# Kernel optimization log

Measured on AMD Instinct MI355X. Metric: run time of the kernel, lower is better.

## Reference

```python
import jax, jax.numpy as jnp
import numpy as np

B, N, F_DIM, E, C = 8, 16384, 64, 262144, 10
BN_EPS = 1e-5


def setup_inputs() -> dict:
    key = jax.random.key(0)
    ks = jax.random.split(key, 10)
    s = 1.0 / np.sqrt(F_DIM)
    return {
        "x": jax.random.normal(ks[0], (B, N, F_DIM), jnp.float32),
        "edge_src": jax.random.randint(ks[1], (B, E), 0, N, jnp.int32),
        "edge_dst": jax.random.randint(ks[2], (B, E), 0, N, jnp.int32),
        "W1": jax.random.normal(ks[3], (F_DIM, F_DIM), jnp.float32) * s,
        "b1": jax.random.normal(ks[4], (F_DIM,), jnp.float32) * 0.01,
        "W2": jax.random.normal(ks[5], (F_DIM, F_DIM), jnp.float32) * s,
        "b2": jax.random.normal(ks[6], (F_DIM,), jnp.float32) * 0.01,
        "bn_gamma": jnp.ones((F_DIM,), jnp.float32),
        "bn_beta": jnp.zeros((F_DIM,), jnp.float32),
        "lin_W": jax.random.normal(ks[7], (C, N * F_DIM), jnp.float32) * (1.0 / np.sqrt(N * F_DIM)),
        "lin_b": jax.random.normal(ks[8], (C,), jnp.float32) * 0.01,
    }


def _graph_conv(x, src, dst, W, b):
    # DGL GraphConv, norm='both', in_feats == out_feats (aggregate-first path):
    # h = D_in^{-1/2} * A * (D_out^{-1/2} * x) @ W + b, degrees clamped to >= 1.
    ones = jnp.ones((src.shape[0],), x.dtype)
    deg_out = jnp.maximum(jax.ops.segment_sum(ones, src, num_segments=N), 1.0)
    deg_in = jnp.maximum(jax.ops.segment_sum(ones, dst, num_segments=N), 1.0)
    xs = x * jax.lax.rsqrt(deg_out)[:, None]          # [N, F]
    agg = jax.ops.segment_sum(xs[src], dst, num_segments=N)  # gather + scatter-add
    rst = agg * jax.lax.rsqrt(deg_in)[:, None]
    return rst @ W + b


def reference(x, edge_src, edge_dst, W1, b1, W2, b2, bn_gamma, bn_beta, lin_W, lin_b):
    conv = jax.vmap(_graph_conv, in_axes=(0, 0, 0, None, None))
    h = jax.nn.relu(conv(x, edge_src, edge_dst, W1, b1))  # conv1 + relu
    # dropout p=0.0 (eval): identity
    h = conv(h, edge_src, edge_dst, W2, b2)               # conv2 -> [B, N, F]
    # BatchNorm1d over channel F (torch normalizes over B and N in training mode)
    mean = jnp.mean(h, axis=(0, 1))
    var = jnp.var(h, axis=(0, 1))
    h = bn_gamma * (h - mean) * jax.lax.rsqrt(var + BN_EPS) + bn_beta
    flat = h.reshape(B, N * F_DIM)
    return flat @ lin_W.T + lin_b                         # [B, C]
```

## Files before the change

### kernel.cpp

```cpp
#include <hip/hip_runtime.h>

#define B_     8
#define N_     16384
#define F_     64
#define E_     262144
#define C_     10
#define NF_    (N_ * F_)
#define BN_    (B_ * N_)
#define BNF_   (B_ * N_ * F_)
#define BE_    (B_ * E_)
#define CAP_   48
#define CHUNK_ 8192
#define NCH_   (E_ / CHUNK_)
#define NW_    (N_ / 4)
#define NSB_   4096
#define NFB_   1024
#define EPS_   1e-5f

typedef _Float16 h8 __attribute__((ext_vector_type(8)));
typedef _Float16 h4 __attribute__((ext_vector_type(4)));
typedef float f32x4 __attribute__((ext_vector_type(4)));

#define SWZ(r, o) ((((r) * 64 + (o))) ^ (((r) & 7) << 3))

__global__ __launch_bounds__(256) void k_count(const int* __restrict__ src,
                                               const int* __restrict__ dst,
                                               unsigned int* __restrict__ partO,
                                               unsigned int* __restrict__ partI,
                                               const float* __restrict__ W1,
                                               const float* __restrict__ W2,
                                               _Float16* __restrict__ Wt1,
                                               _Float16* __restrict__ Wt2) {
    __shared__ unsigned int pO[NW_];
    __shared__ unsigned int pI[NW_];
    int t = threadIdx.x;
    if (blockIdx.x >= B_ * NCH_) {
        int g = blockIdx.x - B_ * NCH_;
        const float* Ws = (g & 8) ? W2 : W1;
        _Float16* Wd = (g & 8) ? Wt2 : Wt1;
        int c0 = (g & 7) * 512;
        for (int j = t; j < 512; j += 256) {
            int o = c0 + j;
            Wd[o] = (_Float16)Ws[(o & 63) * 64 + (o >> 6)];
        }
        return;
    }
    int b = blockIdx.x & 7, c = blockIdx.x >> 3;
    for (int i = t; i < NW_; i += 256) { pO[i] = 0; pI[i] = 0; }
    __syncthreads();
    const int4* sb = (const int4*)(src + (size_t)b * E_ + (size_t)c * CHUNK_);
    const int4* db = (const int4*)(dst + (size_t)b * E_ + (size_t)c * CHUNK_);
#pragma unroll
    for (int j = 0; j < CHUNK_ / 1024; ++j) {
        int4 s4 = sb[t + j * 256];
        int4 d4 = db[t + j * 256];
#pragma unroll
        for (int k = 0; k < 4; ++k) {
            int s = ((const int*)&s4)[k];
            int d = ((const int*)&d4)[k];
            atomicAdd(&pO[s >> 2], 1u << ((s & 3) * 8));
            atomicAdd(&pI[d >> 2], 1u << ((d & 3) * 8));
        }
    }
    __syncthreads();
    size_t base = (size_t)(b * NCH_ + c) * NW_;
    for (int i = t; i < NW_; i += 256) {
        partO[base + i] = pO[i];
        partI[base + i] = pI[i];
    }
}

__global__ __launch_bounds__(256) void k_offsets(const unsigned int* __restrict__ partO,
                                                 const unsigned int* __restrict__ partI,
                                                 unsigned int* __restrict__ baseArr,
                                                 float* __restrict__ degOr,
                                                 float* __restrict__ degIr,
                                                 int* __restrict__ cntI_g) {
    int gw = blockIdx.x * 256 + threadIdx.x;
    int b = gw >> 12;
    int rw = gw & 4095;
    unsigned int sumI = 0, sumO = 0;
#pragma unroll 8
    for (int c = 0; c < NCH_; ++c) {
        size_t idx = (size_t)(b * NCH_ + c) * NW_ + rw;
        unsigned int wI = partI[idx];
        baseArr[idx] = sumI;
        sumI += wI;
        sumO += partO[idx];
    }
    int row0 = gw * 4;
#pragma unroll
    for (int r = 0; r < 4; ++r) {
        unsigned int ci = (sumI >> (r * 8)) & 0xFFu;
        unsigned int co = (sumO >> (r * 8)) & 0xFFu;
        degIr[row0 + r] = rsqrtf(fmaxf((float)ci, 1.0f));
        degOr[row0 + r] = rsqrtf(fmaxf((float)co, 1.0f));
        cntI_g[row0 + r] = (int)ci;
    }
}

__global__ __launch_bounds__(256) void k_fillmm(
        const int* __restrict__ src, const int* __restrict__ dst,
        const unsigned int* __restrict__ baseArr, unsigned short* __restrict__ csr,
        const float* __restrict__ x, const _Float16* __restrict__ Wt,
        const float* __restrict__ rs, _Float16* __restrict__ out) {
    __shared__ char smem[32768];
    int t = threadIdx.x;

    if (blockIdx.x < B_ * NCH_) {
        unsigned int* cur = (unsigned int*)smem;
        unsigned int* bw  = cur + NW_;
        int b = blockIdx.x & 7, c = blockIdx.x >> 3;
        size_t pbase = (size_t)(b * NCH_ + c) * NW_;
        for (int i = t; i < NW_; i += 256) { cur[i] = 0; bw[i] = baseArr[pbase + i]; }
        __syncthreads();
        const int4* sb = (const int4*)(src + (size_t)b * E_ + (size_t)c * CHUNK_);
        const int4* db = (const int4*)(dst + (size_t)b * E_ + (size_t)c * CHUNK_);
        unsigned short* cb = csr + (size_t)b * N_ * CAP_;
#pragma unroll
        for (int j = 0; j < CHUNK_ / 1024; ++j) {
            int4 s4 = sb[t + j * 256];
            int4 d4 = db[t + j * 256];
#pragma unroll
            for (int k = 0; k < 4; ++k) {
                int s = ((const int*)&s4)[k];
                int d = ((const int*)&d4)[k];
                unsigned int sh = (d & 3) * 8;
                unsigned int old = atomicAdd(&cur[d >> 2], 1u << sh);
                unsigned int pos = ((old >> sh) & 0xFFu) + ((bw[d >> 2] >> sh) & 0xFFu);
                if (pos < CAP_) cb[(size_t)d * CAP_ + pos] = (unsigned short)s;
            }
        }
        return;
    }

    _Float16* Al = (_Float16*)smem;
    _Float16* Bl = Al + 4096;
    int g = blockIdx.x - B_ * NCH_;
    int bat = g & 7;
    int rowg = bat * N_ + (g >> 3) * 64;

#pragma unroll
    for (int j = 0; j < 2; ++j) {
        int c = t + j * 256;
        int r = c >> 3, o = (c & 7) * 8;
        *(h8*)&Al[SWZ(r, o)] = *(const h8*)(Wt + c * 8);
    }
#pragma unroll
    for (int j = 0; j < 2; ++j) {
        int c = t + j * 256;
        int r = c >> 3, o = (c & 7) * 8;
        const float4* p = (const float4*)(x + (size_t)(rowg + r) * 64 + o);
        float4 x0 = p[0], x1 = p[1];
        h8 v;
        v[0] = (_Float16)x0.x; v[1] = (_Float16)x0.y;
        v[2] = (_Float16)x0.z; v[3] = (_Float16)x0.w;
        v[4] = (_Float16)x1.x; v[5] = (_Float16)x1.y;
        v[6] = (_Float16)x1.z; v[7] = (_Float16)x1.w;
        *(h8*)&Bl[SWZ(r, o)] = v;
    }
    __syncthreads();

    int lane = t & 63;
    int w = t >> 6;
    int lm = lane & 15;
    int lk = (lane >> 4) * 8;
    f32x4 acc0 = {0.f, 0.f, 0.f, 0.f}, acc1 = {0.f, 0.f, 0.f, 0.f};
    f32x4 acc2 = {0.f, 0.f, 0.f, 0.f}, acc3 = {0.f, 0.f, 0.f, 0.f};
#pragma unroll
    for (int ks = 0; ks < 2; ++ks) {
        h8 a = *(const h8*)&Al[SWZ(w * 16 + lm, lk + ks * 32)];
        h8 vb0 = *(const h8*)&Bl[SWZ(0 + lm, lk + ks * 32)];
        h8 vb1 = *(const h8*)&Bl[SWZ(16 + lm, lk + ks * 32)];
        h8 vb2 = *(const h8*)&Bl[SWZ(32 + lm, lk + ks * 32)];
        h8 vb3 = *(const h8*)&Bl[SWZ(48 + lm, lk + ks * 32)];
        acc0 = __builtin_amdgcn_mfma_f32_16x16x32_f16(a, vb0, acc0, 0, 0, 0);
        acc1 = __builtin_amdgcn_mfma_f32_16x16x32_f16(a, vb1, acc1, 0, 0, 0);
        acc2 = __builtin_amdgcn_mfma_f32_16x16x32_f16(a, vb2, acc2, 0, 0, 0);
        acc3 = __builtin_amdgcn_mfma_f32_16x16x32_f16(a, vb3, acc3, 0, 0, 0);
    }
    int fo = w * 16 + (lane >> 4) * 4;
#define STORE_TILE(ACC, RT)                                                    \
    {                                                                          \
        int row = rowg + (RT) * 16 + lm;                                       \
        float scv = rs[row];                                                   \
        h4 ov;                                                                 \
        ov[0] = (_Float16)(ACC[0] * scv); ov[1] = (_Float16)(ACC[1] * scv);    \
        ov[2] = (_Float16)(ACC[2] * scv); ov[3] = (_Float16)(ACC[3] * scv);    \
        *(h4*)(out + (size_t)row * 64 + fo) = ov;                              \
    }
    STORE_TILE(acc0, 0)
    STORE_TILE(acc1, 1)
    STORE_TILE(acc2, 2)
    STORE_TILE(acc3, 3)
#undef STORE_TILE
}

#define GAT_SEG(KOFF)                                                          \
    {                                                                          \
        int rem = n - (KOFF);                                                  \
        int srcl = lb + ((KOFF) >> 3);                                         \
        unsigned dd0 = __shfl(ev.x, srcl), dd1 = __shfl(ev.y, srcl);           \
        unsigned dd2 = __shfl(ev.z, srcl), dd3 = __shfl(ev.w, srcl);           \
        unsigned dd[4] = {dd0, dd1, dd2, dd3};                                 \
        h8 v[8];                                                               \
        _Pragma("unroll")                                                      \
        for (int jj = 0; jj < 8; ++jj) {                                       \
            int s = (int)((dd[jj >> 1] >> ((jj & 1) * 16)) & 0x3FFFu);         \
            h8 vv = {};                                                        \
            if (jj < rem) vv = *(const h8*)(zb + s * 64 + ho);                 \
            v[jj] = vv;                                                        \
        }                                                                      \
        h8 s0 = v[0] + v[1], s1 = v[2] + v[3];                                 \
        h8 s2 = v[4] + v[5], s3 = v[6] + v[7];                                 \
        h8 s4 = s0 + s1, s5 = s2 + s3;                                         \
        h8 s6 = s4 + s5;                                                       \
        _Pragma("unroll")                                                      \
        for (int i = 0; i < 8; ++i) af[i] += (float)s6[i];                     \
    }

__global__ __launch_bounds__(256, 6) void k_gmm(
        const int* __restrict__ cnt, const unsigned short* __restrict__ csr,
        const _Float16* __restrict__ z, const float* __restrict__ degIr,
        const float* __restrict__ degOr, const float* __restrict__ bias,
        const _Float16* __restrict__ Wt2, _Float16* __restrict__ out) {
    __shared__ _Float16 Al[4096];
    __shared__ _Float16 Bl[2048];
    int t = threadIdx.x;
    int lane = t & 63;
    int wave = t >> 6;
    int c8 = lane & 7;
    int b = blockIdx.x & 7;
    int rl = wave * 8 + (lane >> 3);
    int row0 = (blockIdx.x >> 3) * 32;
    int wid = b * N_ + row0 + rl;
    const _Float16* zb = z + (size_t)b * NF_;
    int lb = lane & 56;
    int ho = c8 * 8;

#pragma unroll
    for (int j = 0; j < 2; ++j) {
        int c = t + j * 256;
        int r = c >> 3, o = (c & 7) * 8;
        *(h8*)&Al[SWZ(r, o)] = *(const h8*)(Wt2 + c * 8);
    }

    int n = cnt[wid];
    if (n > CAP_) n = CAP_;
    size_t cb = (size_t)wid * CAP_;
    uint4 ev = {0u, 0u, 0u, 0u};
    if (c8 * 8 < n) ev = *(const uint4*)(csr + cb + c8 * 8);
    int m = n;
    m = max(m, __shfl_xor(m, 8));
    m = max(m, __shfl_xor(m, 16));
    m = max(m, __shfl_xor(m, 32));

    float af[8];
#pragma unroll
    for (int i = 0; i < 8; ++i) af[i] = 0.0f;
    GAT_SEG(0)
    if (m > 8)  GAT_SEG(8)
    if (m > 16) GAT_SEG(16)
    if (m > 24) GAT_SEG(24)
    if (m > 32) GAT_SEG(32)
    if (m > 40) GAT_SEG(40)

    float dIr = degIr[wid];
    float po = degOr[wid];
    float4 bv0 = *(const float4*)(bias + ho);
    float4 bv1 = *(const float4*)(bias + ho + 4);
    float bb[8] = {bv0.x, bv0.y, bv0.z, bv0.w, bv1.x, bv1.y, bv1.z, bv1.w};
    h8 ov;
#pragma unroll
    for (int i = 0; i < 8; ++i) {
        ov[i] = (_Float16)(fmaxf(fmaf(af[i], dIr, bb[i]), 0.0f) * po);
    }
    *(h8*)&Bl[SWZ(rl, ho)] = ov;
    __syncthreads();

    int lm = lane & 15;
    int lk = (lane >> 4) * 8;
    f32x4 acc0 = {0.f, 0.f, 0.f, 0.f}, acc1 = {0.f, 0.f, 0.f, 0.f};
#pragma unroll
    for (int ks = 0; ks < 2; ++ks) {
        h8 a  = *(const h8*)&Al[SWZ(wave * 16 + lm, lk + ks * 32)];
        h8 v0 = *(const h8*)&Bl[SWZ(lm, lk + ks * 32)];
        h8 v1 = *(const h8*)&Bl[SWZ(16 + lm, lk + ks * 32)];
        acc0 = __builtin_amdgcn_mfma_f32_16x16x32_f16(a, v0, acc0, 0, 0, 0);
        acc1 = __builtin_amdgcn_mfma_f32_16x16x32_f16(a, v1, acc1, 0, 0, 0);
    }
    int fo = wave * 16 + (lane >> 4) * 4;
    int rowg = b * N_ + row0;
    h4 o0, o1;
    o0[0] = (_Float16)acc0[0]; o0[1] = (_Float16)acc0[1];
    o0[2] = (_Float16)acc0[2]; o0[3] = (_Float16)acc0[3];
    o1[0] = (_Float16)acc1[0]; o1[1] = (_Float16)acc1[1];
    o1[2] = (_Float16)acc1[2]; o1[3] = (_Float16)acc1[3];
    *(h4*)(out + (size_t)(rowg + lm) * 64 + fo) = o0;
    *(h4*)(out + (size_t)(rowg + 16 + lm) * 64 + fo) = o1;
}

__global__ __launch_bounds__(256, 6) void k_gat(
        const int* __restrict__ cnt, const unsigned short* __restrict__ csr,
        const _Float16* __restrict__ z, const float* __restrict__ degIr,
        const float* __restrict__ bias, _Float16* __restrict__ out16,
        float* __restrict__ pstat) {
    __shared__ float sS[4][64];
    __shared__ float sQ[4][64];
    int t = threadIdx.x;
    int lane = t & 63;
    int wave = t >> 6;
    int c8 = lane & 7;
    int b = blockIdx.x & 7;
    int row = (blockIdx.x >> 3) * 32 + wave * 8 + (lane >> 3);
    int wid = b * N_ + row;
    const _Float16* zb = z + (size_t)b * NF_;
    int lb = lane & 56;
    int ho = c8 * 8;

    int n = cnt[wid];
    if (n > CAP_) n = CAP_;
    size_t cb = (size_t)wid * CAP_;
    uint4 ev = {0u, 0u, 0u, 0u};
    if (c8 * 8 < n) ev = *(const uint4*)(csr + cb + c8 * 8);
    int m = n;
    m = max(m, __shfl_xor(m, 8));
    m = max(m, __shfl_xor(m, 16));
    m = max(m, __shfl_xor(m, 32));

    float af[8];
#pragma unroll
    for (int i = 0; i < 8; ++i) af[i] = 0.0f;
    GAT_SEG(0)
    if (m > 8)  GAT_SEG(8)
    if (m > 16) GAT_SEG(16)
    if (m > 24) GAT_SEG(24)
    if (m > 32) GAT_SEG(32)
    if (m > 40) GAT_SEG(40)

    float dIr = degIr[wid];
    float4 bv0 = *(const float4*)(bias + ho);
    float4 bv1 = *(const float4*)(bias + ho + 4);
    float bb[8] = {bv0.x, bv0.y, bv0.z, bv0.w, bv1.x, bv1.y, bv1.z, bv1.w};
    float vv[8];
    h8 ov;
#pragma unroll
    for (int i = 0; i < 8; ++i) {
        vv[i] = fmaf(af[i], dIr, bb[i]);
        ov[i] = (_Float16)vv[i];
    }
    *(h8*)(out16 + (size_t)wid * 64 + ho) = ov;
    float ssv[8], qqv[8];
#pragma unroll
    for (int i = 0; i < 8; ++i) { ssv[i] = vv[i]; qqv[i] = vv[i] * vv[i]; }
#pragma unroll
    for (int i = 0; i < 8; ++i) {
        ssv[i] += __shfl_xor(ssv[i], 8);  qqv[i] += __shfl_xor(qqv[i], 8);
        ssv[i] += __shfl_xor(ssv[i], 16); qqv[i] += __shfl_xor(qqv[i], 16);
        ssv[i] += __shfl_xor(ssv[i], 32); qqv[i] += __shfl_xor(qqv[i], 32);
    }
    if (lane < 8) {
#pragma unroll
        for (int i = 0; i < 8; ++i) {
            sS[wave][lane * 8 + i] = ssv[i];
            sQ[wave][lane * 8 + i] = qqv[i];
        }
    }
    __syncthreads();
    if (t < 64) {
        float s_ = sS[0][t] + sS[1][t] + sS[2][t] + sS[3][t];
        float q_ = sQ[0][t] + sQ[1][t] + sQ[2][t] + sQ[3][t];
        pstat[(size_t)blockIdx.x * 128 + t] = s_;
        pstat[(size_t)blockIdx.x * 128 + 64 + t] = q_;
    }
}

__global__ __launch_bounds__(256) void k_red(const float* __restrict__ part,
                                             float* __restrict__ stats2) {
    __shared__ float sred[256];
    int t = threadIdx.x;
    int half = t >> 7;
    int s = t & 127;
    int r0 = blockIdx.x * (NSB_ / 32);
    float acc = 0.0f;
    for (int k = 0; k < NSB_ / 32 / 2; ++k) {
        acc += part[(size_t)(r0 + k * 2 + half) * 128 + s];
    }
    sred[t] = acc;
    __syncthreads();
    if (t < 128) stats2[blockIdx.x * 128 + t] = sred[t] + sred[t + 128];
}

__global__ __launch_bounds__(256) void k_final(
        const _Float16* __restrict__ h, const float* __restrict__ linW,
        const float* __restrict__ stats2, const float* __restrict__ gamma,
        const float* __restrict__ beta, float* __restrict__ pf) {
    __shared__ float pre[256];
    __shared__ float scs[64], shs[64];
    int t = threadIdx.x;
    {
        int u = t & 127, jh = t >> 7;
        float a = 0.0f;
#pragma unroll
        for (int j = 0; j < 16; ++j) a += stats2[(jh * 16 + j) * 128 + u];
        pre[t] = a;
    }
    __syncthreads();
    if (t < 64) {
        float sum = pre[t] + pre[t + 128];
        float sq  = pre[t + 64] + pre[t + 192];
        float inv = 1.0f / (float)BN_;
        float mean = sum * inv;
        float var  = sq * inv - mean * mean;
        float s = gamma[t] * rsqrtf(var + EPS_);
        scs[t] = s;
        shs[t] = beta[t] - mean * s;
    }
    __syncthreads();

    int lane = t & 63;
    int wv = t >> 6;
    int b0 = wv * 2, b1 = wv * 2 + 1;
    int base = blockIdx.x * (NF_ / NFB_);
    float4 s4  = *(const float4*)&scs[(lane & 15) * 4];
    float4 sh4 = *(const float4*)&shs[(lane & 15) * 4];
    float acc[C_][2];
#pragma unroll
    for (int c = 0; c < C_; ++c) { acc[c][0] = 0.0f; acc[c][1] = 0.0f; }

#pragma unroll
    for (int k = 0; k < 4; ++k) {
        int i = base + k * 256 + lane * 4;
        h4 ha = *(const h4*)(h + (size_t)b0 * NF_ + i);
        h4 hb = *(const h4*)(h + (size_t)b1 * NF_ + i);
        float h0[4], h1[4];
        h0[0] = fmaf((float)ha[0], s4.x, sh4.x);
        h0[1] = fmaf((float)ha[1], s4.y, sh4.y);
        h0[2] = fmaf((float)ha[2], s4.z, sh4.z);
        h0[3] = fmaf((float)ha[3], s4.w, sh4.w);
        h1[0] = fmaf((float)hb[0], s4.x, sh4.x);
        h1[1] = fmaf((float)hb[1], s4.y, sh4.y);
        h1[2] = fmaf((float)hb[2], s4.z, sh4.z);
        h1[3] = fmaf((float)hb[3], s4.w, sh4.w);
#pragma unroll
        for (int c = 0; c < C_; ++c) {
            float4 w4 = *(const float4*)(linW + (size_t)c * NF_ + i);
            float a0 = acc[c][0], a1 = acc[c][1];
            a0 = fmaf(h0[0], w4.x, a0); a0 = fmaf(h0[1], w4.y, a0);
            a0 = fmaf(h0[2], w4.z, a0); a0 = fmaf(h0[3], w4.w, a0);
            a1 = fmaf(h1[0], w4.x, a1); a1 = fmaf(h1[1], w4.y, a1);
            a1 = fmaf(h1[2], w4.z, a1); a1 = fmaf(h1[3], w4.w, a1);
            acc[c][0] = a0; acc[c][1] = a1;
        }
    }

#pragma unroll
    for (int c = 0; c < C_; ++c) {
#pragma unroll
        for (int j = 0; j < 2; ++j) {
            float v = acc[c][j];
            v += __shfl_down(v, 32);
            v += __shfl_down(v, 16);
            v += __shfl_down(v, 8);
            v += __shfl_down(v, 4);
            v += __shfl_down(v, 2);
            v += __shfl_down(v, 1);
            acc[c][j] = v;
        }
    }
    if (lane == 0) {
        float* p = pf + (size_t)blockIdx.x * 80;
#pragma unroll
        for (int c = 0; c < C_; ++c) {
            p[b0 * C_ + c] = acc[c][0];
            p[b1 * C_ + c] = acc[c][1];
        }
    }
}

__global__ __launch_bounds__(64) void k_fsum(const float* __restrict__ pf,
                                             const float* __restrict__ linb,
                                             float* __restrict__ out) {
    int o = blockIdx.x;
    int lane = threadIdx.x;
    float acc = 0.0f;
#pragma unroll
    for (int k = 0; k < 16; ++k) {
        acc += pf[(size_t)(k * 64 + lane) * 80 + o];
    }
    acc += __shfl_down(acc, 32);
    acc += __shfl_down(acc, 16);
    acc += __shfl_down(acc, 8);
    acc += __shfl_down(acc, 4);
    acc += __shfl_down(acc, 2);
    acc += __shfl_down(acc, 1);
    if (lane == 0) out[o] = acc + linb[o % C_];
}

extern "C" void kernel_launch(void* const* d_in, const int* in_sizes, int n_in,
                              void* d_out, int out_size, void* d_ws, size_t ws_size,
                              hipStream_t stream) {
    const float* x        = (const float*)d_in[0];
    const int*   edge_src = (const int*)d_in[1];
    const int*   edge_dst = (const int*)d_in[2];
    const float* W1       = (const float*)d_in[3];
    const float* b1       = (const float*)d_in[4];
    const float* W2       = (const float*)d_in[5];
    const float* b2       = (const float*)d_in[6];
    const float* gamma    = (const float*)d_in[7];
    const float* beta     = (const float*)d_in[8];
    const float* linW     = (const float*)d_in[9];
    const float* linb     = (const float*)d_in[10];
    float* out = (float*)d_out;

    char* w = (char*)d_ws;
    float* degOr = (float*)w;           w += BN_ * 4;
    float* degIr = (float*)w;           w += BN_ * 4;
    int*   cntI  = (int*)w;             w += BN_ * 4;
    unsigned short* csr = (unsigned short*)w; w += (size_t)BN_ * CAP_ * 2;
    _Float16* z1   = (_Float16*)w;      w += (size_t)BNF_ * 2;
    _Float16* z2   = (_Float16*)w;      w += (size_t)BNF_ * 2;
    _Float16* h2h  = (_Float16*)w;      w += (size_t)BNF_ * 2;
    unsigned int* partO   = (unsigned int*)w;  w += (size_t)B_ * NCH_ * NW_ * 4;
    unsigned int* partI   = (unsigned int*)w;  w += (size_t)B_ * NCH_ * NW_ * 4;
    unsigned int* baseArr = (unsigned int*)w;  w += (size_t)B_ * NCH_ * NW_ * 4;
    float* partStats = (float*)w;       w += (size_t)NSB_ * 128 * 4;
    float* stats2 = (float*)w;          w += 32 * 128 * 4;
    float* pf    = (float*)w;           w += (size_t)NFB_ * 80 * 4;
    _Float16* Wt1 = (_Float16*)w;       w += 4096 * 2;
    _Float16* Wt2 = (_Float16*)w;       w += 4096 * 2;

    k_count<<<B_ * NCH_ + 16, 256, 0, stream>>>(edge_src, edge_dst, partO, partI,
                                                W1, W2, Wt1, Wt2);
    k_offsets<<<BN_ / 4 / 256, 256, 0, stream>>>(partO, partI, baseArr, degOr, degIr, cntI);

    k_fillmm<<<B_ * NCH_ + BN_ / 64, 256, 0, stream>>>(edge_src, edge_dst, baseArr,
                                                       csr, x, Wt1, degOr, z1);

    k_gmm<<<BN_ / 32, 256, 0, stream>>>(cntI, csr, z1, degIr, degOr, b1, Wt2, z2);
    k_gat<<<BN_ / 32, 256, 0, stream>>>(cntI, csr, z2, degIr, b2, h2h, partStats);

    k_red<<<32, 256, 0, stream>>>(partStats, stats2);
    k_final<<<NFB_, 256, 0, stream>>>(h2h, linW, stats2, gamma, beta, pf);
    k_fsum<<<80, 64, 0, stream>>>(pf, linb, out);
}
```

Measured before the change: 227.6 us.

## Sort nodes by in-degree bucket to balance gather work across waves

Adds 8 extra blocks to the fill kernel that bucket each batch's nodes by in-degree (groups of 8 edges) and write a permutation. The gather-matmul and gather kernels then process rows in permuted order, so lanes within a wave handle nodes with similar neighbor counts and the max-count loop bound wastes fewer iterations. The cost is an indirect row lookup, scattered output writes, and lost locality between neighboring rows.

Measured after the change: 247.3 us. +8.7%, slower.

```diff
diff --git a/kernel.cpp b/kernel.cpp
--- a/kernel.cpp
+++ b/kernel.cpp
@@ -103,7 +103,8 @@
         const int* __restrict__ src, const int* __restrict__ dst,
         const unsigned int* __restrict__ baseArr, unsigned short* __restrict__ csr,
         const float* __restrict__ x, const _Float16* __restrict__ Wt,
-        const float* __restrict__ rs, _Float16* __restrict__ out) {
+        const float* __restrict__ rs, _Float16* __restrict__ out,
+        const int* __restrict__ cntI, unsigned short* __restrict__ perm) {
     __shared__ char smem[32768];
     int t = threadIdx.x;
 
@@ -130,6 +131,34 @@
                 unsigned int pos = ((old >> sh) & 0xFFu) + ((bw[d >> 2] >> sh) & 0xFFu);
                 if (pos < CAP_) cb[(size_t)d * CAP_ + pos] = (unsigned short)s;
             }
+        }
+        return;
+    }
+
+    if (blockIdx.x >= B_ * NCH_ + BN_ / 64) {
+        unsigned char* qa = (unsigned char*)smem;
+        unsigned int* hist = (unsigned int*)(smem + 16384);
+        unsigned int* curq = hist + 8;
+        __shared__ unsigned int basec[8];
+        int g = blockIdx.x - (B_ * NCH_ + BN_ / 64);
+        if (t < 8) { hist[t] = 0; curq[t] = 0; }
+        __syncthreads();
+        for (int i = t; i < N_; i += 256) {
+            int n = cntI[g * N_ + i];
+            int q = (n <= 8) ? 0 : min((n - 1) >> 3, 5);
+            qa[i] = (unsigned char)q;
+            atomicAdd(&hist[q], 1u);
+        }
+        __syncthreads();
+        if (t == 0) {
+            unsigned int acc = 0;
+            for (int q = 0; q < 6; ++q) { basec[q] = acc; acc += hist[q]; }
+        }
+        __syncthreads();
+        for (int i = t; i < N_; i += 256) {
+            int q = qa[i];
+            unsigned int r = atomicAdd(&curq[q], 1u);
+            perm[g * N_ + basec[q] + r] = (unsigned short)i;
         }
         return;
     }
@@ -223,7 +252,8 @@
         const int* __restrict__ cnt, const unsigned short* __restrict__ csr,
         const _Float16* __restrict__ z, const float* __restrict__ degIr,
         const float* __restrict__ degOr, const float* __restrict__ bias,
-        const _Float16* __restrict__ Wt2, _Float16* __restrict__ out) {
+        const _Float16* __restrict__ Wt2, _Float16* __restrict__ out,
+        const unsigned short* __restrict__ perm) {
     __shared__ _Float16 Al[4096];
     __shared__ _Float16 Bl[2048];
     int t = threadIdx.x;
@@ -233,7 +263,8 @@
     int b = blockIdx.x & 7;
     int rl = wave * 8 + (lane >> 3);
     int row0 = (blockIdx.x >> 3) * 32;
-    int wid = b * N_ + row0 + rl;
+    int prow = perm[b * N_ + row0 + rl];
+    int wid = b * N_ + prow;
     const _Float16* zb = z + (size_t)b * NF_;
     int lb = lane & 56;
     int ho = c8 * 8;
@@ -290,21 +321,22 @@
         acc1 = __builtin_amdgcn_mfma_f32_16x16x32_f16(a, v1, acc1, 0, 0, 0);
     }
     int fo = wave * 16 + (lane >> 4) * 4;
-    int rowg = b * N_ + row0;
+    int pr0 = perm[b * N_ + row0 + lm];
+    int pr1 = perm[b * N_ + row0 + 16 + lm];
     h4 o0, o1;
     o0[0] = (_Float16)acc0[0]; o0[1] = (_Float16)acc0[1];
     o0[2] = (_Float16)acc0[2]; o0[3] = (_Float16)acc0[3];
     o1[0] = (_Float16)acc1[0]; o1[1] = (_Float16)acc1[1];
     o1[2] = (_Float16)acc1[2]; o1[3] = (_Float16)acc1[3];
-    *(h4*)(out + (size_t)(rowg + lm) * 64 + fo) = o0;
-    *(h4*)(out + (size_t)(rowg + 16 + lm) * 64 + fo) = o1;
+    *(h4*)(out + ((size_t)b * N_ + pr0) * 64 + fo) = o0;
+    *(h4*)(out + ((size_t)b * N_ + pr1) * 64 + fo) = o1;
 }
 
 __global__ __launch_bounds__(256, 6) void k_gat(
         const int* __restrict__ cnt, const unsigned short* __restrict__ csr,
         const _Float16* __restrict__ z, const float* __restrict__ degIr,
         const float* __restrict__ bias, _Float16* __restrict__ out16,
-        float* __restrict__ pstat) {
+        float* __restrict__ pstat, const unsigned short* __restrict__ perm) {
     __shared__ float sS[4][64];
     __shared__ float sQ[4][64];
     int t = threadIdx.x;
@@ -312,8 +344,9 @@
     int wave = t >> 6;
     int c8 = lane & 7;
     int b = blockIdx.x & 7;
-    int row = (blockIdx.x >> 3) * 32 + wave * 8 + (lane >> 3);
-    int wid = b * N_ + row;
+    int slot = (blockIdx.x >> 3) * 32 + wave * 8 + (lane >> 3);
+    int prow = perm[b * N_ + slot];
+    int wid = b * N_ + prow;
     const _Float16* zb = z + (size_t)b * NF_;
     int lb = lane & 56;
     int ho = c8 * 8;
@@ -529,16 +562,17 @@
     float* pf    = (float*)w;           w += (size_t)NFB_ * 80 * 4;
     _Float16* Wt1 = (_Float16*)w;       w += 4096 * 2;
     _Float16* Wt2 = (_Float16*)w;       w += 4096 * 2;
+    unsigned short* perm = (unsigned short*)w; w += (size_t)BN_ * 2;
 
     k_count<<<B_ * NCH_ + 16, 256, 0, stream>>>(edge_src, edge_dst, partO, partI,
                                                 W1, W2, Wt1, Wt2);
     k_offsets<<<BN_ / 4 / 256, 256, 0, stream>>>(partO, partI, baseArr, degOr, degIr, cntI);
 
-    k_fillmm<<<B_ * NCH_ + BN_ / 64, 256, 0, stream>>>(edge_src, edge_dst, baseArr,
-                                                       csr, x, Wt1, degOr, z1);
-
-    k_gmm<<<BN_ / 32, 256, 0, stream>>>(cntI, csr, z1, degIr, degOr, b1, Wt2, z2);
-    k_gat<<<BN_ / 32, 256, 0, stream>>>(cntI, csr, z2, degIr, b2, h2h, partStats);
+    k_fillmm<<<B_ * NCH_ + BN_ / 64 + 8, 256, 0, stream>>>(edge_src, edge_dst,
+        baseArr, csr, x, Wt1, degOr, z1, cntI, perm);
+
+    k_gmm<<<BN_ / 32, 256, 0, stream>>>(cntI, csr, z1, degIr, degOr, b1, Wt2, z2, perm);
+    k_gat<<<BN_ / 32, 256, 0, stream>>>(cntI, csr, z2, degIr, b2, h2h, partStats, perm);
 
     k_red<<<32, 256, 0, stream>>>(partStats, stats2);
     k_final<<<NFB_, 256, 0, stream>>>(h2h, linW, stats2, gamma, beta, pf);
```

## Pad z buffers with zero sentinel row to drop predicated gathers

Applied to the files above, without the earlier changes.

Pads each batch's z1/z2 feature buffers with extra rows and zeroes row 16448 as a sentinel. A memset fills the unused CSR slots with 0x4040, which the gathers read as that zero row. The gather loops can then load all eight neighbours unconditionally instead of checking each slot against the edge count. Occupancy hints for the two gather kernels are raised from 6 to 8 waves. The trade-off is an extra memset over the whole CSR array each call and fixed loads of unused slots, in exchange for removing per-slot branches and shifts.

Result: no change. 227.5 us (-0.0%).

```diff
diff --git a/kernel.cpp b/kernel.cpp
--- a/kernel.cpp
+++ b/kernel.cpp
@@ -8,7 +8,6 @@
 #define NF_    (N_ * F_)
 #define BN_    (B_ * N_)
 #define BNF_   (B_ * N_ * F_)
-#define BE_    (B_ * E_)
 #define CAP_   48
 #define CHUNK_ 8192
 #define NCH_   (E_ / CHUNK_)
@@ -16,6 +15,9 @@
 #define NSB_   4096
 #define NFB_   1024
 #define EPS_   1e-5f
+#define ZR_    16448
+#define ZROWS_ 16512
+#define ZS_    (ZROWS_ * 64)
 
 typedef _Float16 h8 __attribute__((ext_vector_type(8)));
 typedef _Float16 h4 __attribute__((ext_vector_type(4)));
@@ -30,12 +32,22 @@
                                                const float* __restrict__ W1,
                                                const float* __restrict__ W2,
                                                _Float16* __restrict__ Wt1,
-                                               _Float16* __restrict__ Wt2) {
+                                               _Float16* __restrict__ Wt2,
+                                               _Float16* __restrict__ z1p,
+                                               _Float16* __restrict__ z2p) {
     __shared__ unsigned int pO[NW_];
     __shared__ unsigned int pI[NW_];
     int t = threadIdx.x;
     if (blockIdx.x >= B_ * NCH_) {
         int g = blockIdx.x - B_ * NCH_;
+        if (g == 16) {
+            for (int j = t; j < 512; j += 256) {
+                int bb = j >> 6, i = j & 63;
+                z1p[(size_t)bb * ZS_ + (size_t)ZR_ * 64 + i] = (_Float16)0.0f;
+                z2p[(size_t)bb * ZS_ + (size_t)ZR_ * 64 + i] = (_Float16)0.0f;
+            }
+            return;
+        }
         const float* Ws = (g & 8) ? W2 : W1;
         _Float16* Wd = (g & 8) ? Wt2 : Wt1;
         int c0 = (g & 7) * 512;
@@ -138,7 +150,8 @@
     _Float16* Bl = Al + 4096;
     int g = blockIdx.x - B_ * NCH_;
     int bat = g & 7;
-    int rowg = bat * N_ + (g >> 3) * 64;
+    int r0 = (g >> 3) * 64;
+    _Float16* zo = out + (size_t)bat * ZS_;
 
 #pragma unroll
     for (int j = 0; j < 2; ++j) {
@@ -150,7 +163,7 @@
     for (int j = 0; j < 2; ++j) {
         int c = t + j * 256;
         int r = c >> 3, o = (c & 7) * 8;
-        const float4* p = (const float4*)(x + (size_t)(rowg + r) * 64 + o);
+        const float4* p = (const float4*)(x + ((size_t)bat * N_ + r0 + r) * 64 + o);
         float4 x0 = p[0], x1 = p[1];
         h8 v;
         v[0] = (_Float16)x0.x; v[1] = (_Float16)x0.y;
@@ -182,12 +195,12 @@
     int fo = w * 16 + (lane >> 4) * 4;
 #define STORE_TILE(ACC, RT)                                                    \
     {                                                                          \
-        int row = rowg + (RT) * 16 + lm;                                       \
-        float scv = rs[row];                                                   \
+        int rl = r0 + (RT) * 16 + lm;                                          \
+        float scv = rs[bat * N_ + rl];                                         \
         h4 ov;                                                                 \
         ov[0] = (_Float16)(ACC[0] * scv); ov[1] = (_Float16)(ACC[1] * scv);    \
         ov[2] = (_Float16)(ACC[2] * scv); ov[3] = (_Float16)(ACC[3] * scv);    \
-        *(h4*)(out + (size_t)row * 64 + fo) = ov;                              \
+        *(h4*)(zo + (size_t)rl * 64 + fo) = ov;                                \
     }
     STORE_TILE(acc0, 0)
     STORE_TILE(acc1, 1)
@@ -198,28 +211,23 @@
 
 #define GAT_SEG(KOFF)                                                          \
     {                                                                          \
-        int rem = n - (KOFF);                                                  \
         int srcl = lb + ((KOFF) >> 3);                                         \
-        unsigned dd0 = __shfl(ev.x, srcl), dd1 = __shfl(ev.y, srcl);           \
-        unsigned dd2 = __shfl(ev.z, srcl), dd3 = __shfl(ev.w, srcl);           \
-        unsigned dd[4] = {dd0, dd1, dd2, dd3};                                 \
-        h8 v[8];                                                               \
-        _Pragma("unroll")                                                      \
-        for (int jj = 0; jj < 8; ++jj) {                                       \
-            int s = (int)((dd[jj >> 1] >> ((jj & 1) * 16)) & 0x3FFFu);         \
-            h8 vv = {};                                                        \
-            if (jj < rem) vv = *(const h8*)(zb + s * 64 + ho);                 \
-            v[jj] = vv;                                                        \
-        }                                                                      \
-        h8 s0 = v[0] + v[1], s1 = v[2] + v[3];                                 \
-        h8 s2 = v[4] + v[5], s3 = v[6] + v[7];                                 \
-        h8 s4 = s0 + s1, s5 = s2 + s3;                                         \
-        h8 s6 = s4 + s5;                                                       \
+        unsigned d0 = __shfl(ev.x, srcl), d1 = __shfl(ev.y, srcl);             \
+        unsigned d2 = __shfl(ev.z, srcl), d3 = __shfl(ev.w, srcl);             \
+        h8 v0 = *(const h8*)(zb + (d0 & 0xFFFFu) * 64 + ho);                   \
+        h8 v1 = *(const h8*)(zb + (d0 >> 16) * 64 + ho);                       \
+        h8 v2 = *(const h8*)(zb + (d1 & 0xFFFFu) * 64 + ho);                   \
+        h8 v3 = *(const h8*)(zb + (d1 >> 16) * 64 + ho);                       \
+        h8 v4 = *(const h8*)(zb + (d2 & 0xFFFFu) * 64 + ho);                   \
+        h8 v5 = *(const h8*)(zb + (d2 >> 16) * 64 + ho);                       \
+        h8 v6 = *(const h8*)(zb + (d3 & 0xFFFFu) * 64 + ho);                   \
+        h8 v7 = *(const h8*)(zb + (d3 >> 16) * 64 + ho);                       \
+        h8 s6 = ((v0 + v1) + (v2 + v3)) + ((v4 + v5) + (v6 + v7));             \
         _Pragma("unroll")                                                      \
         for (int i = 0; i < 8; ++i) af[i] += (float)s6[i];                     \
     }
 
-__global__ __launch_bounds__(256, 6) void k_gmm(
+__global__ __launch_bounds__(256, 8) void k_gmm(
         const int* __restrict__ cnt, const unsigned short* __restrict__ csr,
         const _Float16* __restrict__ z, const float* __restrict__ degIr,
         const float* __restrict__ degOr, const float* __restrict__ bias,
@@ -234,7 +242,7 @@
     int rl = wave * 8 + (lane >> 3);
     int row0 = (blockIdx.x >> 3) * 32;
     int wid = b * N_ + row0 + rl;
-    const _Float16* zb = z + (size_t)b * NF_;
+    const _Float16* zb = z + (size_t)b * ZS_;
     int lb = lane & 56;
     int ho = c8 * 8;
 
@@ -249,7 +257,7 @@
     if (n > CAP_) n = CAP_;
     size_t cb = (size_t)wid * CAP_;
     uint4 ev = {0u, 0u, 0u, 0u};
-    if (c8 * 8 < n) ev = *(const uint4*)(csr + cb + c8 * 8);
+    if (c8 < 6) ev = *(const uint4*)(csr + cb + c8 * 8);
     int m = n;
     m = max(m, __shfl_xor(m, 8));
     m = max(m, __shfl_xor(m, 16));
@@ -290,17 +298,17 @@
         acc1 = __builtin_amdgcn_mfma_f32_16x16x32_f16(a, v1, acc1, 0, 0, 0);
     }
     int fo = wave * 16 + (lane >> 4) * 4;
-    int rowg = b * N_ + row0;
+    _Float16* zo = out + (size_t)b * ZS_;
     h4 o0, o1;
     o0[0] = (_Float16)acc0[0]; o0[1] = (_Float16)acc0[1];
     o0[2] = (_Float16)acc0[2]; o0[3] = (_Float16)acc0[3];
     o1[0] = (_Float16)acc1[0]; o1[1] = (_Float16)acc1[1];
     o1[2] = (_Float16)acc1[2]; o1[3] = (_Float16)acc1[3];
-    *(h4*)(out + (size_t)(rowg + lm) * 64 + fo) = o0;
-    *(h4*)(out + (size_t)(rowg + 16 + lm) * 64 + fo) = o1;
-}
-
-__global__ __launch_bounds__(256, 6) void k_gat(
+    *(h4*)(zo + (size_t)(row0 + lm) * 64 + fo) = o0;
+    *(h4*)(zo + (size_t)(row0 + 16 + lm) * 64 + fo) = o1;
+}
+
+__global__ __launch_bounds__(256, 8) void k_gat(
         const int* __restrict__ cnt, const unsigned short* __restrict__ csr,
         const _Float16* __restrict__ z, const float* __restrict__ degIr,
         const float* __restrict__ bias, _Float16* __restrict__ out16,
@@ -314,7 +322,7 @@
     int b = blockIdx.x & 7;
     int row = (blockIdx.x >> 3) * 32 + wave * 8 + (lane >> 3);
     int wid = b * N_ + row;
-    const _Float16* zb = z + (size_t)b * NF_;
+    const _Float16* zb = z + (size_t)b * ZS_;
     int lb = lane & 56;
     int ho = c8 * 8;
 
@@ -322,7 +330,7 @@
     if (n > CAP_) n = CAP_;
     size_t cb = (size_t)wid * CAP_;
     uint4 ev = {0u, 0u, 0u, 0u};
-    if (c8 * 8 < n) ev = *(const uint4*)(csr + cb + c8 * 8);
+    if (c8 < 6) ev = *(const uint4*)(csr + cb + c8 * 8);
     int m = n;
     m = max(m, __shfl_xor(m, 8));
     m = max(m, __shfl_xor(m, 16));
@@ -518,8 +526,8 @@
     float* degIr = (float*)w;           w += BN_ * 4;
     int*   cntI  = (int*)w;             w += BN_ * 4;
     unsigned short* csr = (unsigned short*)w; w += (size_t)BN_ * CAP_ * 2;
-    _Float16* z1   = (_Float16*)w;      w += (size_t)BNF_ * 2;
-    _Float16* z2   = (_Float16*)w;      w += (size_t)BNF_ * 2;
+    _Float16* z1   = (_Float16*)w;      w += (size_t)B_ * ZS_ * 2;
+    _Float16* z2   = (_Float16*)w;      w += (size_t)B_ * ZS_ * 2;
     _Float16* h2h  = (_Float16*)w;      w += (size_t)BNF_ * 2;
     unsigned int* partO   = (unsigned int*)w;  w += (size_t)B_ * NCH_ * NW_ * 4;
     unsigned int* partI   = (unsigned int*)w;  w += (size_t)B_ * NCH_ * NW_ * 4;
@@ -530,8 +538,10 @@
     _Float16* Wt1 = (_Float16*)w;       w += 4096 * 2;
     _Float16* Wt2 = (_Float16*)w;       w += 4096 * 2;
 
-    k_count<<<B_ * NCH_ + 16, 256, 0, stream>>>(edge_src, edge_dst, partO, partI,
-                                                W1, W2, Wt1, Wt2);
+    hipMemsetAsync(csr, 0x40, (size_t)BN_ * CAP_ * 2, stream);
+
+    k_count<<<B_ * NCH_ + 17, 256, 0, stream>>>(edge_src, edge_dst, partO, partI,
+                                                W1, W2, Wt1, Wt2, z1, z2);
     k_offsets<<<BN_ / 4 / 256, 256, 0, stream>>>(partO, partI, baseArr, degOr, degIr, cntI);
 
     k_fillmm<<<B_ * NCH_ + BN_ / 64, 256, 0, stream>>>(edge_src, edge_dst, baseArr,
```
